# Optimization experiments

Hardware: AMD Instinct MI355X
Metric: run time of the kernel (lower is better)

The kernel has to match this reference:

```python
import jax, jax.numpy as jnp
import numpy as np

B, S, T = 32, 64, 64
E, H = 512, 512
V_SRC = 32000
V_TGT = 32000


def setup_inputs() -> dict:
    key = jax.random.key(0)
    ks = jax.random.split(key, 16)
    g = lambda i, shape: jax.random.normal(ks[i], shape, jnp.float32) * 0.05
    return {
        "src_sentences": jax.random.randint(ks[0], (B, S), 0, V_SRC),
        "target_sentences": jax.random.randint(ks[1], (B, T), 0, V_TGT),
        "source_sentence_length": jnp.full((B,), S, dtype=jnp.int32),
        "src_emb": g(2, (V_SRC, E)),
        "tgt_emb": g(3, (V_TGT, E)),
        "enc_Wih_f": g(4, (4 * H, E)), "enc_Whh_f": g(5, (4 * H, H)), "enc_b_f": jnp.zeros((4 * H,), jnp.float32),
        "enc_Wih_b": g(6, (4 * H, E)), "enc_Whh_b": g(7, (4 * H, H)), "enc_b_b": jnp.zeros((4 * H,), jnp.float32),
        "dec_Wih": g(8, (4 * H, E + H)), "dec_Whh": g(9, (4 * H, H)), "dec_b": jnp.zeros((4 * H,), jnp.float32),
        "W_att_src": g(10, (H, 2 * H)),
        "W_att_vec": g(11, (H, 3 * H)),
        "W_readout": g(12, (V_TGT, H)),
        "W_init": g(13, (H, 2 * H)), "b_init": jnp.zeros((H,), jnp.float32),
    }


def _lstm_cell(x, h, c, Wih, Whh, b):
    # PyTorch gate order: i, f, g, o ; b = b_ih + b_hh combined
    gates = x @ Wih.T + h @ Whh.T + b
    i, f, g, o = jnp.split(gates, 4, axis=-1)
    c_new = jax.nn.sigmoid(f) * c + jax.nn.sigmoid(i) * jnp.tanh(g)
    h_new = jax.nn.sigmoid(o) * jnp.tanh(c_new)
    return h_new, c_new


def _enc_dir(xs, lengths, Wih, Whh, b, reverse):
    # xs: [S, B, E]; emulates packed LSTM: state frozen / outputs zero at padded steps
    Sn, Bn, _ = xs.shape
    Hd = Whh.shape[1]
    ts = jnp.arange(Sn)

    def step(carry, inp):
        h, c = carry
        x, t = inp
        valid = (t < lengths)[:, None].astype(x.dtype)  # [B,1]
        h2, c2 = _lstm_cell(x, h, c, Wih, Whh, b)
        h = valid * h2 + (1.0 - valid) * h
        c = valid * c2 + (1.0 - valid) * c
        return (h, c), valid * h

    init = (jnp.zeros((Bn, Hd), xs.dtype), jnp.zeros((Bn, Hd), xs.dtype))
    (hT, cT), outs = jax.lax.scan(step, init, (xs, ts), reverse=reverse)
    return outs, hT, cT


def reference(src_sentences, target_sentences, source_sentence_length,
              src_emb, tgt_emb,
              enc_Wih_f, enc_Whh_f, enc_b_f,
              enc_Wih_b, enc_Whh_b, enc_b_b,
              dec_Wih, dec_Whh, dec_b,
              W_att_src, W_att_vec, W_readout, W_init, b_init):
    Bn, Sn = src_sentences.shape
    Hh = dec_Whh.shape[1]
    # faithful to original: embedding [B,S,E] then .view(S,B,E) (a reshape)
    src_x = src_emb[src_sentences].reshape(Sn, Bn, -1)  # [S,B,E]
    out_f, _, c_f = _enc_dir(src_x, source_sentence_length, enc_Wih_f, enc_Whh_f, enc_b_f, False)
    out_b, _, c_b = _enc_dir(src_x, source_sentence_length, enc_Wih_b, enc_Whh_b, enc_b_b, True)
    src_enc = jnp.concatenate([out_f, out_b], axis=-1).transpose(1, 0, 2)  # [B,S,2H]
    dec_c0 = jnp.concatenate([c_f, c_b], axis=-1) @ W_init.T + b_init
    dec_h0 = jnp.tanh(dec_c0)

    pad_mask = jnp.arange(Sn)[None, :] >= source_sentence_length[:, None]  # [B,S] True = pad
    src_att = src_enc @ W_att_src.T  # [B,S,H]
    ys = tgt_emb[target_sentences].transpose(1, 0, 2)  # [T,B,E]

    def dec_step(carry, y):
        h, c, att = carry
        x = jnp.concatenate([y, att], axis=-1)  # feed_input=True
        h, c = _lstm_cell(x, h, c, dec_Wih, dec_Whh, dec_b)
        score = jnp.einsum('bsh,bh->bs', src_att, h)
        score = jnp.where(pad_mask, -jnp.inf, score)
        alpha = jax.nn.softmax(score, axis=-1)
        ctx = jnp.einsum('bs,bsd->bd', alpha, src_enc)
        att = jnp.tanh(jnp.concatenate([h, ctx], axis=-1) @ W_att_vec.T)
        return (h, c, att), att

    att0 = jnp.zeros((Bn, Hh), src_x.dtype)
    _, att_ves = jax.lax.scan(dec_step, (dec_h0, dec_c0, att0), ys)  # [T,B,H]

    logp = jax.nn.log_softmax(att_ves @ W_readout.T, axis=-1)  # [T,B,V]
    logp = logp.transpose(1, 0, 2)  # [B,T,V]
    gold = jnp.take_along_axis(logp, target_sentences[:, :, None], axis=-1).squeeze(-1)  # [B,T]
    gold = gold * (target_sentences != 0).astype(logp.dtype)
    # faithful to original: permuted to batch-first then sum(dim=0) -> per-timestep sums, shape [T]
    return gold.sum(axis=0)
```

## Files before the change

kernel.cpp:

```cpp
#include <hip/hip_runtime.h>
#include <hip/hip_bf16.h>
#include <cmath>


__device__ __forceinline__ float sigf(float x){ return 1.0f/(1.0f+__expf(-x)); }
__device__ __forceinline__ short f2bf(float x){
    unsigned u = __builtin_bit_cast(unsigned, x);
    u += 0x7fff + ((u >> 16) & 1);
    return (short)(u >> 16);
}

typedef __attribute__((ext_vector_type(8))) short short8;
typedef __attribute__((ext_vector_type(4))) float float4v;

constexpr long o_senc   = 0;
constexpr long o_satt   = o_senc + 32L*64*1024;
constexpr long o_aves   = o_satt + 32L*64*512;
constexpr long o_hF     = o_aves + 64L*32*512;
constexpr long o_cF     = o_hF + 32L*512;
constexpr long o_hB     = o_cF + 32L*512;
constexpr long o_cB     = o_hB + 32L*512;
constexpr long o_sumexp = o_cB + 32L*512;
constexpr long o_gold   = o_sumexp + 2048;
constexpr long o_ccat   = o_gold + 2048;
constexpr long o_dech   = o_ccat + 32L*1024;
constexpr long o_decc   = o_dech + 32L*512;
constexpr long o_att    = o_decc + 32L*512;
constexpr long o_ctx    = o_att + 32L*512;

__device__ __align__(16) float g_X[3][2048L*2048];
__device__ __align__(16) short g_Wread_bf[32000L*512];
__device__ __align__(16) short g_bfA[2][2048L*512];
__device__ __align__(16) short g_bfW[3][2048L*512];
__device__ __align__(16) short g_aves_bf[2048L*512];

__device__ __forceinline__ float ld_devf(const float* p){
    return __hip_atomic_load(p, __ATOMIC_RELAXED, __HIP_MEMORY_SCOPE_AGENT);
}
__device__ __forceinline__ void st_devf(float* p, float v){
    __hip_atomic_store(p, v, __ATOMIC_RELAXED, __HIP_MEMORY_SCOPE_AGENT);
}
__device__ __forceinline__ float2 ld_devf2(const float* p){
    unsigned long long u = __hip_atomic_load((const unsigned long long*)p,
                                             __ATOMIC_RELAXED, __HIP_MEMORY_SCOPE_AGENT);
    return __builtin_bit_cast(float2, u);
}

__device__ __align__(128) unsigned long long g_arr[256][16];
__device__ unsigned long long g_rel = 0ull;

__device__ __forceinline__ unsigned long long ld_flag(const unsigned long long* p){
    return __hip_atomic_load(p, __ATOMIC_RELAXED, __HIP_MEMORY_SCOPE_AGENT);
}
__device__ __forceinline__ void st_flag(unsigned long long* p, unsigned long long v){
    __hip_atomic_store(p, v, __ATOMIC_RELAXED, __HIP_MEMORY_SCOPE_AGENT);
}

__device__ __forceinline__ void gsync(unsigned long long ep){
    asm volatile("s_waitcnt vmcnt(0)" ::: "memory");
    __syncthreads();
    if (blockIdx.x == 0){
        int tid = threadIdx.x;
        if (tid > 0){
            while (ld_flag(&g_arr[tid][0]) < ep)
                __builtin_amdgcn_s_sleep(1);
        }
        __syncthreads();
        if (tid == 0) st_flag(&g_rel, ep);
    } else {
        if (threadIdx.x == 0){
            st_flag(&g_arr[blockIdx.x][0], ep);
            while (ld_flag(&g_rel) < ep)
                __builtin_amdgcn_s_sleep(1);
        }
        __syncthreads();
    }
    asm volatile("" ::: "memory");
}

__global__ void k_zero(float* p, int n){
    int i = blockIdx.x*256 + threadIdx.x;
    if (i < n) p[i] = 0.f;
}

__global__ void k_cvt(const float* __restrict__ in, short* __restrict__ out, int ldin){
    long idx = (long)blockIdx.x*256 + threadIdx.x;
    long r = idx >> 9; int c = idx & 511;
    out[idx] = f2bf(in[r*ldin + c]);
}

__global__ void k_gather_bf(const float* __restrict__ emb, const int* __restrict__ tok,
                            short* __restrict__ out, int mode){
    long idx = (long)blockIdx.x*256 + threadIdx.x;
    int m = idx >> 9, e = idx & 511;
    int ti = mode ? ((m & 31)*64 + (m >> 5)) : m;
    out[idx] = f2bf(emb[(long)tok[ti]*512 + e]);
}

template<int STORE>
__global__ __launch_bounds__(256)
void k_mfma_gemm(const short* __restrict__ A, const short* __restrict__ B,
                 float* __restrict__ C, int ldc){
    __shared__ short As[128][72];
    __shared__ short Bs[128][72];
    int tid = threadIdx.x, l = tid & 63, w = tid >> 6;
    int wm = w >> 1, wn = w & 1;
    long m0 = (long)blockIdx.x * 128, n0 = (long)blockIdx.y * 128;
    float4v acc[4][4];
    #pragma unroll
    for (int a=0;a<4;++a)
        #pragma unroll
        for (int b=0;b<4;++b)
            #pragma unroll
            for (int e=0;e<4;++e) acc[a][b][e] = 0.f;

    for (int kb = 0; kb < 8; ++kb){
        #pragma unroll
        for (int i = tid; i < 1024; i += 256){
            int r = i >> 3, c = i & 7;
            *(uint4*)&As[r][c*8] = *(const uint4*)(A + (m0+r)*512 + kb*64 + c*8);
            *(uint4*)&Bs[r][c*8] = *(const uint4*)(B + (n0+r)*512 + kb*64 + c*8);
        }
        __syncthreads();
        #pragma unroll
        for (int ks = 0; ks < 2; ++ks){
            short8 af[4], bf[4];
            #pragma unroll
            for (int tm=0;tm<4;++tm)
                af[tm] = *(const short8*)&As[wm*64 + tm*16 + (l&15)][ks*32 + (l>>4)*8];
            #pragma unroll
            for (int tn=0;tn<4;++tn)
                bf[tn] = *(const short8*)&Bs[wn*64 + tn*16 + (l&15)][ks*32 + (l>>4)*8];
            #pragma unroll
            for (int tm=0;tm<4;++tm)
                #pragma unroll
                for (int tn=0;tn<4;++tn)
                    acc[tm][tn] = __builtin_amdgcn_mfma_f32_16x16x32_bf16(
                        af[tm], bf[tn], acc[tm][tn], 0, 0, 0);
        }
        __syncthreads();
    }

    int q = l >> 4;
    if (STORE){
        #pragma unroll
        for (int tm=0;tm<4;++tm)
            #pragma unroll
            for (int r=0;r<4;++r){
                long m = m0 + wm*64 + tm*16 + q*4 + r;
                #pragma unroll
                for (int tn=0;tn<4;++tn)
                    C[m*ldc + n0 + wn*64 + tn*16 + (l&15)] = acc[tm][tn][r];
            }
    } else {
        #pragma unroll
        for (int tm=0;tm<4;++tm)
            #pragma unroll
            for (int r=0;r<4;++r){
                float s = 0.f;
                #pragma unroll
                for (int tn=0;tn<4;++tn) s += __expf(acc[tm][tn][r]);
                s += __shfl_xor(s, 1); s += __shfl_xor(s, 2);
                s += __shfl_xor(s, 4); s += __shfl_xor(s, 8);
                if ((l & 15) == 0)
                    atomicAdd(&C[m0 + wm*64 + tm*16 + q*4 + r], s);
            }
    }
}

__global__ __launch_bounds__(256, 1)
void k_encoder(const float* __restrict__ WhhF, const float* __restrict__ WhhB,
               const float* __restrict__ bF, const float* __restrict__ bB,
               const int* __restrict__ lens,
               float* __restrict__ hF, float* __restrict__ cF,
               float* __restrict__ hB, float* __restrict__ cB,
               float* __restrict__ senc)
{
    __shared__ float WS[16][516];
    __shared__ float xS[32][516];
    __shared__ float gS[32][16];

    const int bid = blockIdx.x, tid = threadIdx.x;
    const int dir = bid >> 7, jg = bid & 127;
    const int j0 = jg * 4;
    const float* Whh  = dir ? WhhB : WhhF;
    const float* bias = dir ? bB : bF;
    const float* X = g_X[dir];
    float* hPtr = dir ? hB : hF;

    for (int i = tid; i < 2048; i += 256){
        int nn = i >> 7, c4 = i & 127;
        int n = (nn >> 2)*512 + j0 + (nn & 3);
        *(float4*)&WS[nn][c4*4] = *(const float4*)(Whh + (long)n*512 + c4*4);
    }

    const int nn = tid & 15, b2 = tid >> 4;
    const int cb = tid >> 2, cjj = tid & 3;
    const int len_b = lens[cb & 31];
    float c_reg = 0.f, h_reg = 0.f;

    unsigned long long ep = ld_flag(&g_rel);

    for (int s = 0; s < 64; ++s){
        if (s){
            ep++; gsync(ep);
            for (int i = tid; i < 8192; i += 256){
                float2 v = ld_devf2(hPtr + i*2);
                xS[i >> 8][(i & 255)*2]     = v.x;
                xS[i >> 8][(i & 255)*2 + 1] = v.y;
            }
        }
        __syncthreads();
        float p[4] = {0.f,0.f,0.f,0.f}, q[4] = {0.f,0.f,0.f,0.f};
        if (s){
            const float* wr = &WS[nn][0];
            const float* xa = &xS[b2][0];
            const float* xb = &xS[b2 + 16][0];
            #pragma unroll 2
            for (int k = 0; k < 512; k += 16){
                #pragma unroll
                for (int u = 0; u < 4; ++u){
                    float4 w = *(const float4*)(wr + k + u*4);
                    float4 a = *(const float4*)(xa + k + u*4);
                    float4 b = *(const float4*)(xb + k + u*4);
                    p[u] += w.x*a.x + w.y*a.y + w.z*a.z + w.w*a.w;
                    q[u] += w.x*b.x + w.y*b.y + w.z*b.z + w.w*b.w;
                }
            }
        }
        gS[b2][nn]    = p[0]+p[1]+p[2]+p[3];
        gS[b2+16][nn] = q[0]+q[1]+q[2]+q[3];
        __syncthreads();
        if (tid < 128){
            int sd = dir ? 63 - s : s;
            int j = j0 + cjj;
            const float* xr = X + ((long)(sd*32 + cb))*2048;
            float g0 = gS[cb][cjj]      + xr[j]      + bias[j];
            float g1 = gS[cb][4 + cjj]  + xr[512+j]  + bias[512+j];
            float g2 = gS[cb][8 + cjj]  + xr[1024+j] + bias[1024+j];
            float g3 = gS[cb][12 + cjj] + xr[1536+j] + bias[1536+j];
            float cn = sigf(g1)*c_reg + sigf(g0)*tanhf(g2);
            float hn = sigf(g3)*tanhf(cn);
            bool valid = sd < len_b;
            c_reg = valid ? cn : c_reg;
            h_reg = valid ? hn : h_reg;
            st_devf(hPtr + cb*512 + j, h_reg);
            senc[((long)(cb*64 + sd))*1024 + dir*512 + j] = valid ? hn : 0.f;
        }
    }
    if (tid < 128){
        float* cOut = dir ? cB : cF;
        cOut[cb*512 + j0 + cjj] = c_reg;
    }
}

__global__ __launch_bounds__(256, 1)
void k_decoder(const float* __restrict__ dWhh, const float* __restrict__ dWih,
               const float* __restrict__ db, const float* __restrict__ Wv,
               const float* __restrict__ satt, const float* __restrict__ senc,
               const int* __restrict__ lens,
               float* __restrict__ dech, const float* __restrict__ decc,
               float* __restrict__ attG, float* __restrict__ ctxG,
               float* __restrict__ aves)
{
    __shared__ float xS[32][516];
    __shared__ float WdS[8][1028];
    __shared__ float WvS[4][1540];
    __shared__ float gS[32][8];
    __shared__ float scoreQ[64][5];
    __shared__ float alphaS[64];
    __shared__ float ctxP[2][128];

    const int bid = blockIdx.x, tid = threadIdx.x;
    const float* Yg = g_X[2];

    {
        int j0 = bid*2;
        for (int i = tid; i < 2048; i += 256){
            int nn = i >> 8, c4 = i & 255;
            int n = (nn >> 1)*512 + j0 + (nn & 1);
            float4 v;
            if (c4 < 128) v = *(const float4*)(dWhh + (long)n*512  + c4*4);
            else          v = *(const float4*)(dWih + (long)n*1024 + 512 + (c4-128)*4);
            *(float4*)&WdS[nn][c4*4] = v;
        }
        if (bid < 128){
            for (int i = tid; i < 1536; i += 256){
                int r = i / 384, c4 = i % 384;
                *(float4*)&WvS[r][c4*4] = *(const float4*)(Wv + (long)(bid*4+r)*1536 + c4*4);
            }
        }
    }

    float c_reg = 0.f;
    if (tid < 64) c_reg = decc[(tid>>1)*512 + bid*2 + (tid&1)];

    const int nnA = tid & 7, bA = tid >> 3;
    unsigned long long ep = ld_flag(&g_rel);

    for (int t = 0; t < 64; ++t){
        if (t == 0 || bid >= 128){
            for (int i = tid; i < 8192; i += 256){
                float2 v = ld_devf2(dech + i*2);
                xS[i >> 8][(i & 255)*2]     = v.x;
                xS[i >> 8][(i & 255)*2 + 1] = v.y;
            }
        }
        __syncthreads();
        float p[4] = {0.f,0.f,0.f,0.f};
        {
            const float* wr = &WdS[nnA][0];
            const float* xr = &xS[bA][0];
            #pragma unroll 2
            for (int k = 0; k < 512; k += 16){
                #pragma unroll
                for (int u = 0; u < 4; ++u){
                    float4 w = *(const float4*)(wr + k + u*4);
                    float4 a = *(const float4*)(xr + k + u*4);
                    p[u] += w.x*a.x + w.y*a.y + w.z*a.z + w.w*a.w;
                }
            }
        }

        if (t){ ep++; gsync(ep); }

        if (t){
            for (int i = tid; i < 8192; i += 256){
                float2 v = ld_devf2(attG + i*2);
                xS[i >> 8][(i & 255)*2]     = v.x;
                xS[i >> 8][(i & 255)*2 + 1] = v.y;
            }
            __syncthreads();
            const float* wr = &WdS[nnA][512];
            const float* xr = &xS[bA][0];
            #pragma unroll 2
            for (int k = 0; k < 512; k += 16){
                #pragma unroll
                for (int u = 0; u < 4; ++u){
                    float4 w = *(const float4*)(wr + k + u*4);
                    float4 a = *(const float4*)(xr + k + u*4);
                    p[u] += w.x*a.x + w.y*a.y + w.z*a.z + w.w*a.w;
                }
            }
        }
        gS[bA][nnA] = p[0]+p[1]+p[2]+p[3];
        __syncthreads();
        if (tid < 64){
            int b = tid >> 1, jj = tid & 1, j = bid*2 + jj;
            const float* yr = Yg + ((long)t*32 + b)*2048;
            float g0 = gS[b][0 + jj] + yr[j]      + db[j];
            float g1 = gS[b][2 + jj] + yr[512+j]  + db[512+j];
            float g2 = gS[b][4 + jj] + yr[1024+j] + db[1024+j];
            float g3 = gS[b][6 + jj] + yr[1536+j] + db[1536+j];
            float cn = sigf(g1)*c_reg + sigf(g0)*tanhf(g2);
            float hn = sigf(g3)*tanhf(cn);
            c_reg = cn;
            st_devf(dech + b*512 + j, hn);
        }
        ep++; gsync(ep);

        {
            int bb = bid >> 3, cs = bid & 7;
            float* hBS = &xS[0][0];
            {
                float2 v = ld_devf2(dech + bb*512 + tid*2);
                hBS[tid*2] = v.x; hBS[tid*2 + 1] = v.y;
            }
            __syncthreads();
            {
                int ss = tid >> 2, qq = tid & 3;
                const float* sar = satt + ((long)(bb*64 + ss))*512 + qq*128;
                const float* hr = hBS + qq*128;
                float u[4] = {0.f,0.f,0.f,0.f};
                #pragma unroll 2
                for (int k = 0; k < 128; k += 16){
                    #pragma unroll
                    for (int u4 = 0; u4 < 4; ++u4){
                        float4 a = *(const float4*)(sar + k + u4*4);
                        float4 h = *(const float4*)(hr  + k + u4*4);
                        u[u4] += a.x*h.x + a.y*h.y + a.z*h.z + a.w*h.w;
                    }
                }
                scoreQ[ss][qq] = u[0]+u[1]+u[2]+u[3];
            }
            __syncthreads();
            if (tid < 64){
                float sc = scoreQ[tid][0]+scoreQ[tid][1]+scoreQ[tid][2]+scoreQ[tid][3];
                if (tid >= lens[bb]) sc = -INFINITY;
                float mx = sc;
                #pragma unroll
                for (int o=32;o>0;o>>=1) mx = fmaxf(mx, __shfl_xor(mx, o));
                float e = (sc == -INFINITY) ? 0.f : __expf(sc - mx);
                float sm = e;
                #pragma unroll
                for (int o=32;o>0;o>>=1) sm += __shfl_xor(sm, o);
                alphaS[tid] = e / fmaxf(sm, 1e-30f);
            }
            __syncthreads();
            {
                int cc = tid & 127, sh = tid >> 7;
                const float* sb = senc + ((long)bb*64 + sh*32)*1024 + cs*128 + cc;
                float a0 = 0.f, a1 = 0.f;
                for (int s2 = 0; s2 < 32; s2 += 2){
                    a0 += alphaS[sh*32 + s2]     * sb[(long)s2*1024];
                    a1 += alphaS[sh*32 + s2 + 1] * sb[(long)(s2+1)*1024];
                }
                ctxP[sh][cc] = a0 + a1;
            }
            __syncthreads();
            if (tid < 128)
                st_devf(ctxG + (bid>>3)*1024 + (bid&7)*128 + tid,
                        ctxP[0][tid] + ctxP[1][tid]);
        }
        ep++; gsync(ep);

        if (bid < 128){
            int b3 = tid >> 3, nv = (tid >> 1) & 3, kq = tid & 1;
            float q[4] = {0.f,0.f,0.f,0.f};
            const int chord[3] = {1, 2, 0};
            #pragma unroll
            for (int ci = 0; ci < 3; ++ci){
                int ch = chord[ci];
                __syncthreads();
                for (int i = tid; i < 8192; i += 256){
                    float2 v;
                    if (ch == 0) v = ld_devf2(dech + i*2);
                    else         v = ld_devf2(ctxG + (long)(i>>8)*1024 + (ch-1)*512 + (i&255)*2);
                    xS[i >> 8][(i & 255)*2]     = v.x;
                    xS[i >> 8][(i & 255)*2 + 1] = v.y;
                }
                __syncthreads();
                const float* xr = &xS[b3][kq*256];
                const float* wr = &WvS[nv][ch*512 + kq*256];
                #pragma unroll 2
                for (int k = 0; k < 256; k += 16){
                    #pragma unroll
                    for (int u = 0; u < 4; ++u){
                        float4 w = *(const float4*)(wr + k + u*4);
                        float4 a = *(const float4*)(xr + k + u*4);
                        q[u] += w.x*a.x + w.y*a.y + w.z*a.z + w.w*a.w;
                    }
                }
            }
            float acc = q[0]+q[1]+q[2]+q[3];
            acc += __shfl_xor(acc, 1);
            if (kq == 0){
                float v = tanhf(acc);
                int n = bid*4 + nv;
                st_devf(attG + b3*512 + n, v);
                long m = (long)t*32 + b3;
                aves[m*512 + n] = v;
                g_aves_bf[m*512 + n] = f2bf(v);
            }
        }
    }
}

__global__ void k_ccat(const float* __restrict__ cF, const float* __restrict__ cB,
                       float* __restrict__ ccat){
    int idx = blockIdx.x*256 + threadIdx.x;
    int b = idx >> 10, d = idx & 1023;
    ccat[idx] = (d < 512) ? cF[b*512+d] : cB[b*512+d-512];
}

__global__ __launch_bounds__(256)
void k_gemm(const float* __restrict__ A, const float* __restrict__ W,
            const float* __restrict__ bias, float* __restrict__ C,
            int M, int K, int lda, int ldw, int ldc){
    __shared__ float As[16][65];
    __shared__ float Wt[16][65];
    int tid = threadIdx.x;
    int m0 = blockIdx.x * 64, n0 = blockIdx.y * 64;
    int ty = tid >> 4, tx = tid & 15;
    int lm = tid >> 2, lk = (tid & 3) * 4;
    float acc[4][4] = {};
    for (int kt = 0; kt < K; kt += 16){
        float4 av;
        if (m0 + lm < M) av = *(const float4*)(A + (long)(m0+lm)*lda + kt + lk);
        else av = make_float4(0.f,0.f,0.f,0.f);
        As[lk+0][lm]=av.x; As[lk+1][lm]=av.y; As[lk+2][lm]=av.z; As[lk+3][lm]=av.w;
        float4 wv = *(const float4*)(W + (long)(n0+lm)*ldw + kt + lk);
        Wt[lk+0][lm]=wv.x; Wt[lk+1][lm]=wv.y; Wt[lk+2][lm]=wv.z; Wt[lk+3][lm]=wv.w;
        __syncthreads();
        #pragma unroll
        for (int k = 0; k < 16; ++k){
            float a0=As[k][ty*4+0], a1=As[k][ty*4+1], a2=As[k][ty*4+2], a3=As[k][ty*4+3];
            float b0=Wt[k][tx*4+0], b1=Wt[k][tx*4+1], b2=Wt[k][tx*4+2], b3=Wt[k][tx*4+3];
            acc[0][0]+=a0*b0; acc[0][1]+=a0*b1; acc[0][2]+=a0*b2; acc[0][3]+=a0*b3;
            acc[1][0]+=a1*b0; acc[1][1]+=a1*b1; acc[1][2]+=a1*b2; acc[1][3]+=a1*b3;
            acc[2][0]+=a2*b0; acc[2][1]+=a2*b1; acc[2][2]+=a2*b2; acc[2][3]+=a2*b3;
            acc[3][0]+=a3*b0; acc[3][1]+=a3*b1; acc[3][2]+=a3*b2; acc[3][3]+=a3*b3;
        }
        __syncthreads();
    }
    #pragma unroll
    for (int i=0;i<4;++i){
        int m = m0 + ty*4 + i;
        if (m >= M) continue;
        #pragma unroll
        for (int j=0;j<4;++j){
            int n = n0 + tx*4 + j;
            float v = acc[i][j];
            if (bias) v += bias[n];
            C[(long)m*ldc + n] = v;
        }
    }
}

__global__ void k_dec_init(const float* __restrict__ decc0, float* dech){
    int idx = blockIdx.x*256 + threadIdx.x;
    dech[idx] = tanhf(decc0[idx]);
}

__global__ void k_gold(const float* __restrict__ aves, const float* __restrict__ Wr,
                       const int* __restrict__ tgt, float* __restrict__ gold){
    int wid = threadIdx.x >> 6, lane = threadIdx.x & 63;
    int m = blockIdx.x*4 + wid;
    int t = m >> 5, b = m & 31;
    int g = tgt[b*64 + t];
    const float* arow = aves + (long)m*512;
    const float* wrow = Wr + (long)g*512;
    float p = 0.f;
    for (int k=lane; k<512; k+=64) p += arow[k]*wrow[k];
    #pragma unroll
    for (int o=32;o>0;o>>=1) p += __shfl_xor(p, o);
    if (lane == 0) gold[m] = p;
}

__global__ void k_final(const float* __restrict__ gold, const float* __restrict__ sumexp,
                        const int* __restrict__ tgt, float* __restrict__ out){
    int t = threadIdx.x;
    float a = 0.f;
    for (int b=0;b<32;++b){
        int m = t*32 + b;
        float lp = gold[m] - logf(fmaxf(sumexp[m], 1e-30f));
        if (tgt[b*64 + t] != 0) a += lp;
    }
    out[t] = a;
}

extern "C" void kernel_launch(void* const* d_in, const int* in_sizes, int n_in,
                              void* d_out, int out_size, void* d_ws, size_t ws_size,
                              hipStream_t stream){
    const int* src_tok   = (const int*)d_in[0];
    const int* tgt_tok   = (const int*)d_in[1];
    const int* lens      = (const int*)d_in[2];
    const float* src_emb = (const float*)d_in[3];
    const float* tgt_emb = (const float*)d_in[4];
    const float* eWihF   = (const float*)d_in[5];
    const float* eWhhF   = (const float*)d_in[6];
    const float* ebF     = (const float*)d_in[7];
    const float* eWihB   = (const float*)d_in[8];
    const float* eWhhB   = (const float*)d_in[9];
    const float* ebB     = (const float*)d_in[10];
    const float* dWih    = (const float*)d_in[11];
    const float* dWhh    = (const float*)d_in[12];
    const float* db      = (const float*)d_in[13];
    const float* Wasrc   = (const float*)d_in[14];
    const float* Wavec   = (const float*)d_in[15];
    const float* Wread   = (const float*)d_in[16];
    const float* Winit   = (const float*)d_in[17];
    const float* binit   = (const float*)d_in[18];
    float* ws  = (float*)d_ws;
    float* out = (float*)d_out;

    float* senc = ws + o_senc;  float* satt = ws + o_satt; float* aves = ws + o_aves;
    float* hF = ws + o_hF; float* cF = ws + o_cF; float* hB = ws + o_hB; float* cB = ws + o_cB;
    float* sumexp = ws + o_sumexp; float* gold = ws + o_gold;
    float* ccat = ws + o_ccat;
    float* dech = ws + o_dech; float* decc = ws + o_decc;
    float* attG = ws + o_att; float* ctxG = ws + o_ctx;

    float* Xf; short *WreadBf, *srcxBf, *tgtyBf, *WihFbf, *WihBbf, *dWihYbf;
    hipGetSymbolAddress((void**)&Xf, HIP_SYMBOL(g_X));
    hipGetSymbolAddress((void**)&WreadBf, HIP_SYMBOL(g_Wread_bf));
    hipGetSymbolAddress((void**)&srcxBf, HIP_SYMBOL(g_bfA));
    hipGetSymbolAddress((void**)&WihFbf, HIP_SYMBOL(g_bfW));
    tgtyBf = srcxBf + 2048L*512;
    WihBbf = WihFbf + 2048L*512;
    dWihYbf = WihFbf + 2L*2048*512;

    k_zero<<<264, 256, 0, stream>>>(hF, 67584);

    k_cvt<<<4096, 256, 0, stream>>>(eWihF, WihFbf, 512);
    k_cvt<<<4096, 256, 0, stream>>>(eWihB, WihBbf, 512);
    k_cvt<<<4096, 256, 0, stream>>>(dWih, dWihYbf, 1024);
    k_cvt<<<64000, 256, 0, stream>>>(Wread, WreadBf, 512);
    k_gather_bf<<<4096, 256, 0, stream>>>(src_emb, src_tok, srcxBf, 0);
    k_gather_bf<<<4096, 256, 0, stream>>>(tgt_emb, tgt_tok, tgtyBf, 1);

    k_mfma_gemm<1><<<dim3(16,16), 256, 0, stream>>>(srcxBf, WihFbf, Xf, 2048);
    k_mfma_gemm<1><<<dim3(16,16), 256, 0, stream>>>(srcxBf, WihBbf, Xf + 2048L*2048, 2048);
    k_mfma_gemm<1><<<dim3(16,16), 256, 0, stream>>>(tgtyBf, dWihYbf, Xf + 2L*2048*2048, 2048);

    k_encoder<<<256, 256, 0, stream>>>(eWhhF, eWhhB, ebF, ebB, lens, hF, cF, hB, cB, senc);

    k_ccat<<<128, 256, 0, stream>>>(cF, cB, ccat);
    k_gemm<<<dim3(32,8), 256, 0, stream>>>(senc, Wasrc, nullptr, satt, 2048, 1024, 1024, 1024, 512);
    k_gemm<<<dim3(1,8), 256, 0, stream>>>(ccat, Winit, binit, decc, 32, 1024, 1024, 1024, 512);
    k_dec_init<<<64, 256, 0, stream>>>(decc, dech);

    k_decoder<<<256, 256, 0, stream>>>(dWhh, dWih, db, Wavec, satt, senc, lens,
                                       dech, decc, attG, ctxG, aves);

    short* avesBf; hipGetSymbolAddress((void**)&avesBf, HIP_SYMBOL(g_aves_bf));
    k_mfma_gemm<0><<<dim3(16,250), 256, 0, stream>>>(avesBf, WreadBf, sumexp, 0);
    k_gold<<<512, 256, 0, stream>>>(aves, Wread, tgt_tok, gold);
    k_final<<<1, 64, 0, stream>>>(gold, sumexp, tgt_tok, out);
}
```

Measured before the change: 5.185 ms.

## Precompute context projection through W_att_vec and drop one decoder grid sync per step

Uses linearity to precompute sv = src_enc @ W_att_vec[:,H:].T once as a GEMM before the decoder. Each step then needs only alpha·sv plus h·W_att_vec[:, :H] per block, which removes the ctx round-trip through global memory and one grid-wide barrier per timestep. The release flag of the grid barrier is also spread over eight cache lines to reduce contention while blocks poll. In exchange there is an extra 2048x1024x512 GEMM, W_att_vec rows are read from global memory every step instead of from shared memory, and all blocks now reload dech every step.

```diff
diff --git a/kernel.cpp b/kernel.cpp
--- a/kernel.cpp
+++ b/kernel.cpp
@@ -26,7 +26,7 @@
 constexpr long o_dech   = o_ccat + 32L*1024;
 constexpr long o_decc   = o_dech + 32L*512;
 constexpr long o_att    = o_decc + 32L*512;
-constexpr long o_ctx    = o_att + 32L*512;
+constexpr long o_sv     = o_att + 32L*512;
 
 __device__ __align__(16) float g_X[3][2048L*2048];
 __device__ __align__(16) short g_Wread_bf[32000L*512];
@@ -47,7 +47,7 @@
 }
 
 __device__ __align__(128) unsigned long long g_arr[256][16];
-__device__ unsigned long long g_rel = 0ull;
+__device__ __align__(128) unsigned long long g_relA[8][16];
 
 __device__ __forceinline__ unsigned long long ld_flag(const unsigned long long* p){
     return __hip_atomic_load(p, __ATOMIC_RELAXED, __HIP_MEMORY_SCOPE_AGENT);
@@ -66,11 +66,11 @@
                 __builtin_amdgcn_s_sleep(1);
         }
         __syncthreads();
-        if (tid == 0) st_flag(&g_rel, ep);
+        if (tid < 8) st_flag(&g_relA[tid][0], ep);
     } else {
         if (threadIdx.x == 0){
             st_flag(&g_arr[blockIdx.x][0], ep);
-            while (ld_flag(&g_rel) < ep)
+            while (ld_flag(&g_relA[blockIdx.x & 7][0]) < ep)
                 __builtin_amdgcn_s_sleep(1);
         }
         __syncthreads();
@@ -199,7 +199,7 @@
     const int len_b = lens[cb & 31];
     float c_reg = 0.f, h_reg = 0.f;
 
-    unsigned long long ep = ld_flag(&g_rel);
+    unsigned long long ep = ld_flag(&g_relA[0][0]);
 
     for (int s = 0; s < 64; ++s){
         if (s){
@@ -257,19 +257,19 @@
 __global__ __launch_bounds__(256, 1)
 void k_decoder(const float* __restrict__ dWhh, const float* __restrict__ dWih,
                const float* __restrict__ db, const float* __restrict__ Wv,
-               const float* __restrict__ satt, const float* __restrict__ senc,
+               const float* __restrict__ satt, const float* __restrict__ sv,
                const int* __restrict__ lens,
                float* __restrict__ dech, const float* __restrict__ decc,
-               float* __restrict__ attG, float* __restrict__ ctxG,
-               float* __restrict__ aves)
+               float* __restrict__ attG, float* __restrict__ aves)
 {
     __shared__ float xS[32][516];
     __shared__ float WdS[8][1028];
-    __shared__ float WvS[4][1540];
     __shared__ float gS[32][8];
+    __shared__ float hS[512];
     __shared__ float scoreQ[64][5];
+    __shared__ float hpQ[64][5];
     __shared__ float alphaS[64];
-    __shared__ float ctxP[2][128];
+    __shared__ float svP[4][68];
 
     const int bid = blockIdx.x, tid = threadIdx.x;
     const float* Yg = g_X[2];
@@ -284,27 +284,22 @@
             else          v = *(const float4*)(dWih + (long)n*1024 + 512 + (c4-128)*4);
             *(float4*)&WdS[nn][c4*4] = v;
         }
-        if (bid < 128){
-            for (int i = tid; i < 1536; i += 256){
-                int r = i / 384, c4 = i % 384;
-                *(float4*)&WvS[r][c4*4] = *(const float4*)(Wv + (long)(bid*4+r)*1536 + c4*4);
-            }
-        }
     }
 
     float c_reg = 0.f;
     if (tid < 64) c_reg = decc[(tid>>1)*512 + bid*2 + (tid&1)];
 
     const int nnA = tid & 7, bA = tid >> 3;
-    unsigned long long ep = ld_flag(&g_rel);
+    const int cb = bid >> 3, cn0 = (bid & 7) * 64;
+    const int clen = lens[cb];
+
+    unsigned long long ep = ld_flag(&g_relA[0][0]);
 
     for (int t = 0; t < 64; ++t){
-        if (t == 0 || bid >= 128){
-            for (int i = tid; i < 8192; i += 256){
-                float2 v = ld_devf2(dech + i*2);
-                xS[i >> 8][(i & 255)*2]     = v.x;
-                xS[i >> 8][(i & 255)*2 + 1] = v.y;
-            }
+        for (int i = tid; i < 8192; i += 256){
+            float2 v = ld_devf2(dech + i*2);
+            xS[i >> 8][(i & 255)*2]     = v.x;
+            xS[i >> 8][(i & 255)*2 + 1] = v.y;
         }
         __syncthreads();
         float p[4] = {0.f,0.f,0.f,0.f};
@@ -322,9 +317,8 @@
             }
         }
 
-        if (t){ ep++; gsync(ep); }
-
         if (t){
+            ep++; gsync(ep);
             for (int i = tid; i < 8192; i += 256){
                 float2 v = ld_devf2(attG + i*2);
                 xS[i >> 8][(i & 255)*2]     = v.x;
@@ -360,98 +354,62 @@
         ep++; gsync(ep);
 
         {
-            int bb = bid >> 3, cs = bid & 7;
-            float* hBS = &xS[0][0];
-            {
-                float2 v = ld_devf2(dech + bb*512 + tid*2);
-                hBS[tid*2] = v.x; hBS[tid*2 + 1] = v.y;
-            }
-            __syncthreads();
-            {
-                int ss = tid >> 2, qq = tid & 3;
-                const float* sar = satt + ((long)(bb*64 + ss))*512 + qq*128;
-                const float* hr = hBS + qq*128;
-                float u[4] = {0.f,0.f,0.f,0.f};
-                #pragma unroll 2
-                for (int k = 0; k < 128; k += 16){
-                    #pragma unroll
-                    for (int u4 = 0; u4 < 4; ++u4){
-                        float4 a = *(const float4*)(sar + k + u4*4);
-                        float4 h = *(const float4*)(hr  + k + u4*4);
-                        u[u4] += a.x*h.x + a.y*h.y + a.z*h.z + a.w*h.w;
-                    }
+            float2 v = ld_devf2(dech + cb*512 + tid*2);
+            hS[tid*2] = v.x; hS[tid*2 + 1] = v.y;
+        }
+        __syncthreads();
+        {
+            int rr = tid >> 2, q = tid & 3;
+            const float* sar = satt + ((long)(cb*64 + rr))*512 + q*128;
+            const float* wvr = Wv + (long)(cn0 + rr)*1536 + q*128;
+            const float* hr  = hS + q*128;
+            float us[4] = {0.f,0.f,0.f,0.f}, uw[4] = {0.f,0.f,0.f,0.f};
+            #pragma unroll 2
+            for (int k = 0; k < 128; k += 16){
+                #pragma unroll
+                for (int u = 0; u < 4; ++u){
+                    float4 h = *(const float4*)(hr  + k + u*4);
+                    float4 a = *(const float4*)(sar + k + u*4);
+                    float4 w = *(const float4*)(wvr + k + u*4);
+                    us[u] += a.x*h.x + a.y*h.y + a.z*h.z + a.w*h.w;
+                    uw[u] += w.x*h.x + w.y*h.y + w.z*h.z + w.w*h.w;
                 }
-                scoreQ[ss][qq] = u[0]+u[1]+u[2]+u[3];
-            }
-            __syncthreads();
-            if (tid < 64){
-                float sc = scoreQ[tid][0]+scoreQ[tid][1]+scoreQ[tid][2]+scoreQ[tid][3];
-                if (tid >= lens[bb]) sc = -INFINITY;
-                float mx = sc;
-                #pragma unroll
-                for (int o=32;o>0;o>>=1) mx = fmaxf(mx, __shfl_xor(mx, o));
-                float e = (sc == -INFINITY) ? 0.f : __expf(sc - mx);
-                float sm = e;
-                #pragma unroll
-                for (int o=32;o>0;o>>=1) sm += __shfl_xor(sm, o);
-                alphaS[tid] = e / fmaxf(sm, 1e-30f);
-            }
-            __syncthreads();
-            {
-                int cc = tid & 127, sh = tid >> 7;
-                const float* sb = senc + ((long)bb*64 + sh*32)*1024 + cs*128 + cc;
-                float a0 = 0.f, a1 = 0.f;
-                for (int s2 = 0; s2 < 32; s2 += 2){
-                    a0 += alphaS[sh*32 + s2]     * sb[(long)s2*1024];
-                    a1 += alphaS[sh*32 + s2 + 1] * sb[(long)(s2+1)*1024];
-                }
-                ctxP[sh][cc] = a0 + a1;
-            }
-            __syncthreads();
-            if (tid < 128)
-                st_devf(ctxG + (bid>>3)*1024 + (bid&7)*128 + tid,
-                        ctxP[0][tid] + ctxP[1][tid]);
-        }
-        ep++; gsync(ep);
-
-        if (bid < 128){
-            int b3 = tid >> 3, nv = (tid >> 1) & 3, kq = tid & 1;
-            float q[4] = {0.f,0.f,0.f,0.f};
-            const int chord[3] = {1, 2, 0};
-            #pragma unroll
-            for (int ci = 0; ci < 3; ++ci){
-                int ch = chord[ci];
-                __syncthreads();
-                for (int i = tid; i < 8192; i += 256){
-                    float2 v;
-                    if (ch == 0) v = ld_devf2(dech + i*2);
-                    else         v = ld_devf2(ctxG + (long)(i>>8)*1024 + (ch-1)*512 + (i&255)*2);
-                    xS[i >> 8][(i & 255)*2]     = v.x;
-                    xS[i >> 8][(i & 255)*2 + 1] = v.y;
-                }
-                __syncthreads();
-                const float* xr = &xS[b3][kq*256];
-                const float* wr = &WvS[nv][ch*512 + kq*256];
-                #pragma unroll 2
-                for (int k = 0; k < 256; k += 16){
-                    #pragma unroll
-                    for (int u = 0; u < 4; ++u){
-                        float4 w = *(const float4*)(wr + k + u*4);
-                        float4 a = *(const float4*)(xr + k + u*4);
-                        q[u] += w.x*a.x + w.y*a.y + w.z*a.z + w.w*a.w;
-                    }
-                }
-            }
-            float acc = q[0]+q[1]+q[2]+q[3];
-            acc += __shfl_xor(acc, 1);
-            if (kq == 0){
-                float v = tanhf(acc);
-                int n = bid*4 + nv;
-                st_devf(attG + b3*512 + n, v);
-                long m = (long)t*32 + b3;
-                aves[m*512 + n] = v;
-                g_aves_bf[m*512 + n] = f2bf(v);
-            }
+            }
+            scoreQ[rr][q] = us[0]+us[1]+us[2]+us[3];
+            hpQ[rr][q]    = uw[0]+uw[1]+uw[2]+uw[3];
+        }
+        __syncthreads();
+        if (tid < 64){
+            float sc = scoreQ[tid][0]+scoreQ[tid][1]+scoreQ[tid][2]+scoreQ[tid][3];
+            if (tid >= clen) sc = -INFINITY;
+            float mx = sc;
+            #pragma unroll
+            for (int o=32;o>0;o>>=1) mx = fmaxf(mx, __shfl_xor(mx, o));
+            float e = (sc == -INFINITY) ? 0.f : __expf(sc - mx);
+            float sm = e;
+            #pragma unroll
+            for (int o=32;o>0;o>>=1) sm += __shfl_xor(sm, o);
+            alphaS[tid] = e / fmaxf(sm, 1e-30f);
+        }
+        __syncthreads();
+        {
+            int n = tid & 63, part = tid >> 6;
+            const float* svp = sv + ((long)(cb*64 + part*16))*512 + cn0 + n;
+            float sp = 0.f;
+            #pragma unroll
+            for (int i2 = 0; i2 < 16; ++i2)
+                sp += alphaS[part*16 + i2] * svp[(long)i2*512];
+            svP[part][n] = sp;
+        }
+        __syncthreads();
+        if (tid < 64){
+            float val = hpQ[tid][0]+hpQ[tid][1]+hpQ[tid][2]+hpQ[tid][3]
+                      + svP[0][tid]+svP[1][tid]+svP[2][tid]+svP[3][tid];
+            float v = tanhf(val);
+            st_devf(attG + cb*512 + cn0 + tid, v);
+            long m = (long)t*32 + cb;
+            aves[m*512 + cn0 + tid] = v;
+            g_aves_bf[m*512 + cn0 + tid] = f2bf(v);
         }
     }
 }
@@ -569,7 +527,7 @@
     float* sumexp = ws + o_sumexp; float* gold = ws + o_gold;
     float* ccat = ws + o_ccat;
     float* dech = ws + o_dech; float* decc = ws + o_decc;
-    float* attG = ws + o_att; float* ctxG = ws + o_ctx;
+    float* attG = ws + o_att; float* sv = ws + o_sv;
 
     float* Xf; short *WreadBf, *srcxBf, *tgtyBf, *WihFbf, *WihBbf, *dWihYbf;
     hipGetSymbolAddress((void**)&Xf, HIP_SYMBOL(g_X));
@@ -597,11 +555,12 @@
 
     k_ccat<<<128, 256, 0, stream>>>(cF, cB, ccat);
     k_gemm<<<dim3(32,8), 256, 0, stream>>>(senc, Wasrc, nullptr, satt, 2048, 1024, 1024, 1024, 512);
+    k_gemm<<<dim3(32,8), 256, 0, stream>>>(senc, Wavec + 512, nullptr, sv, 2048, 1024, 1024, 1536, 512);
     k_gemm<<<dim3(1,8), 256, 0, stream>>>(ccat, Winit, binit, decc, 32, 1024, 1024, 1024, 512);
     k_dec_init<<<64, 256, 0, stream>>>(decc, dech);
 
-    k_decoder<<<256, 256, 0, stream>>>(dWhh, dWih, db, Wavec, satt, senc, lens,
-                                       dech, decc, attG, ctxG, aves);
+    k_decoder<<<256, 256, 0, stream>>>(dWhh, dWih, db, Wavec, satt, sv, lens,
+                                       dech, decc, attG, aves);
 
     short* avesBf; hipGetSymbolAddress((void**)&avesBf, HIP_SYMBOL(g_aves_bf));
     k_mfma_gemm<0><<<dim3(16,250), 256, 0, stream>>>(avesBf, WreadBf, sumexp, 0);
```

Result: faster. 4.155 ms (-19.9%).
